# Optimization experiments

Measured on AMD Instinct MI355X. Metric: run time of the kernel, lower is better.

The kernel has to match this reference:

```python
import jax, jax.numpy as jnp
import numpy as np

N, C_IN, C_OUT, HID, H = 4096, 512, 512, 128, 4
HEAD_OUT = C_OUT // H  # 128
MID = 4 * C_OUT        # 2048
R = 1.0                # spatial radius r
L = 48                 # sequence window l
NEG = -1e9


def layer_norm(x, g, b, eps=1e-5):
    m = jnp.mean(x, axis=-1, keepdims=True)
    v = jnp.mean(jnp.square(x - m), axis=-1, keepdims=True)
    return (x - m) * jax.lax.rsqrt(v + eps) * g + b


def setup_inputs() -> dict:
    key = jax.random.key(0)
    ks = jax.random.split(key, 16)
    s = lambda fan: 1.0 / np.sqrt(fan)
    return {
        "x":   jax.random.normal(ks[0], (N, C_IN), jnp.float32),
        "pos": jax.random.normal(ks[1], (N, 3), jnp.float32),
        "ori": jax.random.normal(ks[2], (N, 3), jnp.float32),
        "seq": jnp.arange(N, dtype=jnp.int64) if jax.config.jax_enable_x64 else jnp.arange(N, dtype=jnp.int32),
        "batch": jnp.sort(jax.random.randint(ks[3], (N,), 0, 8)),
        "ln1_g": jnp.ones((C_IN,), jnp.float32),
        "ln1_b": jnp.zeros((C_IN,), jnp.float32),
        "ln2_g": jnp.ones((C_OUT,), jnp.float32),
        "ln2_b": jnp.zeros((C_OUT,), jnp.float32),
        "Wq": jax.random.normal(ks[4], (H, C_IN, HID), jnp.float32) * s(C_IN),
        "Wk": jax.random.normal(ks[5], (H, C_IN, HID), jnp.float32) * s(C_IN),
        "Wv": jax.random.normal(ks[6], (H, C_IN, HID), jnp.float32) * s(C_IN),
        "Wo": jax.random.normal(ks[7], (H, HID, HEAD_OUT), jnp.float32) * s(HID),
        "lnm_g": jnp.ones((MID,), jnp.float32),
        "lnm_b": jnp.zeros((MID,), jnp.float32),
        "W1": jax.random.normal(ks[8], (C_OUT, MID), jnp.float32) * s(C_OUT),
        "W2": jax.random.normal(ks[9], (MID, C_OUT), jnp.float32) * s(MID),
    }


def _block(x, pos, ori, seq, batch, ln1_g, ln1_b, ln2_g, ln2_b,
           Wq, Wk, Wv, Wo, lnm_g, lnm_b, W1, W2):
    identity = x
    xn = layer_norm(x, ln1_g, ln1_b)

    # geometry/sequence neighborhood mask: same graph, ||dp||<=r, |ds|<=l
    d2 = jnp.sum(jnp.square(pos[:, None, :] - pos[None, :, :]), axis=-1)  # [N,N]
    ds = jnp.abs(seq[:, None] - seq[None, :])
    mask = (batch[:, None] == batch[None, :]) & (d2 <= R * R) & (ds <= L)

    # all heads at once (original loops over heads; math identical)
    q = jnp.einsum('nc,hcd->hnd', xn, Wq)
    k = jnp.einsum('nc,hcd->hnd', xn, Wk)
    v = jnp.einsum('nc,hcd->hnd', xn, Wv)
    gbias = ori @ ori.T  # geometric orientation bias [N,N]
    scores = jnp.einsum('hnd,hmd->hnm', q, k) / np.sqrt(HID) + gbias[None]
    scores = jnp.where(mask[None], scores, NEG)
    attn = jax.nn.softmax(scores, axis=-1)
    o = jnp.einsum('hnm,hmd->hnd', attn, v)
    o = jnp.einsum('hnd,hde->hne', o, Wo)               # [H,N,HEAD_OUT]
    o = jnp.transpose(o, (1, 0, 2)).reshape(N, C_OUT)   # concat heads

    x = o + identity
    identity = x
    h = layer_norm(x, ln2_g, ln2_b) @ W1
    h = jax.nn.relu(layer_norm(h, lnm_g, lnm_b))
    return h @ W2 + identity


def reference(x, pos, ori, seq, batch, ln1_g, ln1_b, ln2_g, ln2_b,
              Wq, Wk, Wv, Wo, lnm_g, lnm_b, W1, W2):
    return _block(x, pos, ori, seq, batch, ln1_g, ln1_b, ln2_g, ln2_b,
                  Wq, Wk, Wv, Wo, lnm_g, lnm_b, W1, W2)
```

## Files before the change

kernel.cpp:

```cpp
#include <hip/hip_runtime.h>

typedef unsigned short u16;
typedef unsigned int u32;
typedef float f32x4 __attribute__((ext_vector_type(4)));
typedef __bf16 bf16x8 __attribute__((ext_vector_type(8)));

#define N_TOK 4096
#define QKV_LD 1536
#define NH 4
#define HID 128
#define C_OUT 512

__device__ __forceinline__ float b2f(u16 u) { return __uint_as_float(((u32)u) << 16); }
__device__ __forceinline__ u16 f2b(float f) {
  u32 u = __float_as_uint(f);
  u32 r = (u + 0x7fffu + ((u >> 16) & 1u)) >> 16;
  return (u16)r;
}

__device__ __forceinline__ void gload16(const u16* g, u16* l) {
  __builtin_amdgcn_global_load_lds(
      (const __attribute__((address_space(1))) void*)g,
      (__attribute__((address_space(3))) void*)l, 16, 0, 0);
}

__device__ __forceinline__ void tr32(const float* __restrict__ s,
                                     u16* __restrict__ d, int R, int C,
                                     int r0, int c0, u16 (*tile)[33]) {
  const int tx = threadIdx.x & 31, ty = threadIdx.x >> 5;
#pragma unroll
  for (int i = 0; i < 32; i += 8)
    tile[ty + i][tx] = f2b(s[(size_t)(r0 + ty + i) * C + c0 + tx]);
  __syncthreads();
#pragma unroll
  for (int i = 0; i < 32; i += 8)
    d[(size_t)(c0 + ty + i) * R + r0 + tx] = tile[tx][ty + i];
}

__device__ __forceinline__ void tr32_512(const float* __restrict__ s,
                                         u16* __restrict__ d, int R, int C,
                                         int r0, int c0, u16 (*tile)[33]) {
  const int tx = threadIdx.x & 31, ty = threadIdx.x >> 5;
#pragma unroll
  for (int i = 0; i < 32; i += 16)
    tile[ty + i][tx] = f2b(s[(size_t)(r0 + ty + i) * C + c0 + tx]);
  __syncthreads();
#pragma unroll
  for (int i = 0; i < 32; i += 16)
    d[(size_t)(c0 + ty + i) * R + r0 + tx] = tile[tx][ty + i];
}

__device__ __forceinline__ void ln512_body(
    const float* __restrict__ x, const float* __restrict__ g,
    const float* __restrict__ b, u16* __restrict__ y, int row) {
  const int lane = threadIdx.x & 63;
  const float* xr = x + (size_t)row * 512;
  const int c = lane * 8;
  float4 a0 = *(const float4*)(xr + c);
  float4 a1 = *(const float4*)(xr + c + 4);
  float v[8] = {a0.x, a0.y, a0.z, a0.w, a1.x, a1.y, a1.z, a1.w};
  float s1 = 0.f, s2 = 0.f;
#pragma unroll
  for (int i = 0; i < 8; i++) { s1 += v[i]; s2 += v[i] * v[i]; }
#pragma unroll
  for (int o = 32; o; o >>= 1) { s1 += __shfl_xor(s1, o); s2 += __shfl_xor(s2, o); }
  float mean = s1 * (1.f / 512.f);
  float var = s2 * (1.f / 512.f) - mean * mean;
  float rs = rsqrtf(fmaxf(var, 0.f) + 1e-5f);
  float4 g0 = *(const float4*)(g + c), g1 = *(const float4*)(g + c + 4);
  float4 b0 = *(const float4*)(b + c), b1 = *(const float4*)(b + c + 4);
  float gg[8] = {g0.x, g0.y, g0.z, g0.w, g1.x, g1.y, g1.z, g1.w};
  float bb[8] = {b0.x, b0.y, b0.z, b0.w, b1.x, b1.y, b1.z, b1.w};
  u16 t[8];
#pragma unroll
  for (int i = 0; i < 8; i++) t[i] = f2b((v[i] - mean) * rs * gg[i] + bb[i]);
  *(uint4*)(y + (size_t)row * 512 + c) = *(const uint4*)t;
}

__global__ __launch_bounds__(256) void prep(
    const float* __restrict__ x, const float* __restrict__ ln1g,
    const float* __restrict__ ln1b, u16* __restrict__ xn,
    const float* __restrict__ Wq, const float* __restrict__ Wk,
    const float* __restrict__ Wv, const float* __restrict__ Wo,
    const float* __restrict__ W1,
    u16* __restrict__ Btqkv, u16* __restrict__ Wot, u16* __restrict__ W1t)
{
  __shared__ u16 tile[32][33];
  const int bid = blockIdx.x;
  if (bid < 1024) {
    ln512_body(x, ln1g, ln1b, xn, bid * 4 + (threadIdx.x >> 6));
    return;
  }
  const int idx = bid - 1024;
  const float* s; u16* d; int R, C, r0, c0;
  if (idx < 1024) {
    s = W1; d = W1t; R = 512; C = 2048;
    r0 = (idx >> 6) * 32; c0 = (idx & 63) * 32;
  } else if (idx < 1792) {
    int i = idx - 1024;
    int z = i >> 6, rem = i & 63;
    int which = z >> 2, b = z & 3;
    const float* base = (which == 0) ? Wq : (which == 1) ? Wk : Wv;
    s = base + (size_t)b * 512 * 128;
    d = Btqkv + (size_t)which * 4 * 512 * 128 + (size_t)b * 512 * 128;
    R = 512; C = 128;
    r0 = (rem >> 2) * 32; c0 = (rem & 3) * 32;
  } else {
    int i = idx - 1792;
    int b = i >> 4, rem = i & 15;
    s = Wo + (size_t)b * 128 * 128;
    d = Wot + (size_t)b * 128 * 128;
    R = 128; C = 128;
    r0 = (rem >> 2) * 32; c0 = (rem & 3) * 32;
  }
  tr32(s, d, R, C, r0, c0, tile);
}

__global__ __launch_bounds__(256) void ln512_f32(
    const float* __restrict__ x, const float* __restrict__ g,
    const float* __restrict__ b, u16* __restrict__ y)
{
  ln512_body(x, g, b, y, blockIdx.x * 4 + (threadIdx.x >> 6));
}

__global__ __launch_bounds__(256) void ln2048_bf16_relu(
    const u16* __restrict__ x, const float* __restrict__ g,
    const float* __restrict__ b, u16* __restrict__ y)
{
  const int row = blockIdx.x, tid = threadIdx.x;
  const int c = tid * 8;
  const u16* xr = x + (size_t)row * 2048;
  uint4 u = *(const uint4*)(xr + c);
  u16 e[8]; *(uint4*)e = u;
  float v[8];
#pragma unroll
  for (int i = 0; i < 8; i++) v[i] = b2f(e[i]);
  float s1 = 0.f, s2 = 0.f;
#pragma unroll
  for (int i = 0; i < 8; i++) { s1 += v[i]; s2 += v[i] * v[i]; }
#pragma unroll
  for (int o = 32; o; o >>= 1) { s1 += __shfl_xor(s1, o); s2 += __shfl_xor(s2, o); }
  __shared__ float red[2][4];
  int lane = tid & 63, w = tid >> 6;
  if (lane == 0) { red[0][w] = s1; red[1][w] = s2; }
  __syncthreads();
  s1 = red[0][0] + red[0][1] + red[0][2] + red[0][3];
  s2 = red[1][0] + red[1][1] + red[1][2] + red[1][3];
  float mean = s1 * (1.f / 2048.f);
  float var = s2 * (1.f / 2048.f) - mean * mean;
  float rs = rsqrtf(fmaxf(var, 0.f) + 1e-5f);
  float4 g0 = *(const float4*)(g + c), g1 = *(const float4*)(g + c + 4);
  float4 b0 = *(const float4*)(b + c), b1 = *(const float4*)(b + c + 4);
  float gg[8] = {g0.x, g0.y, g0.z, g0.w, g1.x, g1.y, g1.z, g1.w};
  float bb[8] = {b0.x, b0.y, b0.z, b0.w, b1.x, b1.y, b1.z, b1.w};
  u16 t[8];
#pragma unroll
  for (int i = 0; i < 8; i++)
    t[i] = f2b(fmaxf((v[i] - mean) * rs * gg[i] + bb[i], 0.f));
  *(uint4*)(y + (size_t)row * 2048 + c) = *(const uint4*)t;
}

__global__ __launch_bounds__(512, 4) void gemm128(
    const u16* __restrict__ A, int lda,
    const u16* __restrict__ Bt,
    void* __restrict__ C, int ldc, int outf32,
    const float* __restrict__ res,
    int Kslice, int Ktot, int atomic)
{
  __shared__ u16 As[2][128 * 64];
  __shared__ u16 Bs[2][128 * 64];
  const int id = blockIdx.x + gridDim.x * blockIdx.y;
  const int xr = id & 7, xj = id >> 3;
  const int bm = xr * 4 + (xj & 3);
  const int bn = xj >> 2;
  const int m0 = bm * 128, n0 = bn * 128;
  const int kbase = blockIdx.z * Kslice;
  const int tid = threadIdx.x;
  const int lane = tid & 63, w = tid >> 6;
  const int wm = (w & 1) * 64;
  const int wn = (w >> 1) * 32;
  const int l16 = lane & 15, quad = lane >> 4;

  const int sr = tid >> 3;
  const int sch = (tid & 7) ^ (sr & 7);
  const u16* PA = A + (size_t)(m0 + sr) * lda + kbase + sch * 8;
  const u16* PB = Bt + (size_t)(n0 + sr) * Ktot + kbase + sch * 8;
  const size_t askip = (size_t)64 * lda;
  const size_t bskip = (size_t)64 * Ktot;

  f32x4 acc[4][2];
#pragma unroll
  for (int i = 0; i < 4; i++)
#pragma unroll
    for (int j = 0; j < 2; j++) acc[i][j] = (f32x4){0.f, 0.f, 0.f, 0.f};

  {
    gload16(PA, &As[0][w * 512]);
    gload16(PA + askip, &As[0][4096 + w * 512]);
    gload16(PB, &Bs[0][w * 512]);
    gload16(PB + bskip, &Bs[0][4096 + w * 512]);
  }
  __syncthreads();

  int buf = 0;
  for (int kk = 0; kk < Kslice; kk += 64) {
    if (kk + 64 < Kslice) {
      PA += 64; PB += 64;
      gload16(PA, &As[buf ^ 1][w * 512]);
      gload16(PA + askip, &As[buf ^ 1][4096 + w * 512]);
      gload16(PB, &Bs[buf ^ 1][w * 512]);
      gload16(PB + bskip, &Bs[buf ^ 1][4096 + w * 512]);
    }
#pragma unroll
    for (int kc = 0; kc < 2; kc++) {
      bf16x8 af[4], bfr[2];
#pragma unroll
      for (int mt = 0; mt < 4; mt++) {
        int row = wm + mt * 16 + l16;
        af[mt] = *(const bf16x8*)&As[buf][row * 64 + (((kc * 4 + quad) ^ (row & 7)) * 8)];
      }
#pragma unroll
      for (int nt = 0; nt < 2; nt++) {
        int row = wn + nt * 16 + l16;
        bfr[nt] = *(const bf16x8*)&Bs[buf][row * 64 + (((kc * 4 + quad) ^ (row & 7)) * 8)];
      }
#pragma unroll
      for (int mt = 0; mt < 4; mt++)
#pragma unroll
        for (int nt = 0; nt < 2; nt++)
          acc[mt][nt] = __builtin_amdgcn_mfma_f32_16x16x32_bf16(
              af[mt], bfr[nt], acc[mt][nt], 0, 0, 0);
    }
    __syncthreads();
    buf ^= 1;
  }

#pragma unroll
  for (int mt = 0; mt < 4; mt++)
#pragma unroll
    for (int nt = 0; nt < 2; nt++)
#pragma unroll
      for (int r = 0; r < 4; r++) {
        int gr = m0 + wm + mt * 16 + quad * 4 + r;
        int gc = n0 + wn + nt * 16 + l16;
        size_t off = (size_t)gr * ldc + gc;
        float v = acc[mt][nt][r];
        if (atomic) {
          atomicAdd((float*)C + off, v);
        } else {
          if (res) v += res[off];
          if (outf32) ((float*)C)[off] = v;
          else        ((u16*)C)[off] = f2b(v);
        }
      }
}

#define TQ 32
#define BAND 128
#define KROW 136
#define PROW 132
__global__ __launch_bounds__(512) void attn_mfma(
    const u16* __restrict__ qkv, const float* __restrict__ pos,
    const float* __restrict__ ori, const int* __restrict__ batch,
    const u16* __restrict__ wot, const float* __restrict__ xres,
    float* __restrict__ out,
    const float* __restrict__ W2, u16* __restrict__ W2t)
{
  __shared__ u16 kv[128 * KROW];
  __shared__ u16 qp[TQ * KROW];
  __shared__ float ps[TQ * PROW];
  __shared__ float bpx[BAND], bpy[BAND], bpz[BAND];
  __shared__ float box_[BAND], boy_[BAND], boz_[BAND];
  __shared__ int bb[BAND];

  if (blockIdx.x >= 128) {
    int idx = (blockIdx.x - 128) + blockIdx.y * 256;
    int r0 = (idx >> 4) * 32, c0 = (idx & 15) * 32;
    tr32_512(W2, W2t, 2048, 512, r0, c0, (u16(*)[33])kv);
    return;
  }

  const int h = blockIdx.y;
  const int bxs = (blockIdx.x & 7) * 16 + (blockIdx.x >> 3);
  const int i0 = bxs * TQ;
  const int j0 = i0 - 48;
  const int tid = threadIdx.x;
  const int lane = tid & 63, w = tid >> 6;
  const int l16 = lane & 15, quad = lane >> 4;

  if (tid < BAND) {
    int t = tid, j = j0 + t;
    if (j >= 0 && j < N_TOK) {
      bpx[t] = pos[j * 3 + 0]; bpy[t] = pos[j * 3 + 1]; bpz[t] = pos[j * 3 + 2];
      box_[t] = ori[j * 3 + 0]; boy_[t] = ori[j * 3 + 1]; boz_[t] = ori[j * 3 + 2];
      bb[t] = batch[j];
    } else {
      bpx[t] = bpy[t] = bpz[t] = 0.f;
      box_[t] = boy_[t] = boz_[t] = 0.f;
      bb[t] = -12345;
    }
  }
  for (int idx = tid; idx < BAND * 16; idx += 512) {
    int t = idx >> 4, c8 = (idx & 15) * 8;
    int j = j0 + t;
    int4 val = {0, 0, 0, 0};
    if (j >= 0 && j < N_TOK)
      val = *(const int4*)&qkv[(size_t)j * QKV_LD + 512 + h * HID + c8];
    *(int4*)&kv[t * KROW + c8] = val;
  }
  {
    int q = tid >> 4, c8 = (tid & 15) * 8;
    *(int4*)&qp[q * KROW + c8] =
        *(const int4*)&qkv[(size_t)(i0 + q) * QKV_LD + h * HID + c8];
  }
  __syncthreads();

  {
    bf16x8 bf[4];
#pragma unroll
    for (int kc = 0; kc < 4; kc++)
      bf[kc] = *(const bf16x8*)&kv[(w * 16 + l16) * KROW + kc * 32 + quad * 8];
    const int t = w * 16 + l16;
#pragma unroll
    for (int qt = 0; qt < 2; qt++) {
      bf16x8 af[4];
#pragma unroll
      for (int kc = 0; kc < 4; kc++)
        af[kc] = *(const bf16x8*)&qp[(qt * 16 + l16) * KROW + kc * 32 + quad * 8];
      f32x4 acc = (f32x4){0.f, 0.f, 0.f, 0.f};
#pragma unroll
      for (int kc = 0; kc < 4; kc++)
        acc = __builtin_amdgcn_mfma_f32_16x16x32_bf16(af[kc], bf[kc], acc, 0, 0, 0);
#pragma unroll
      for (int r = 0; r < 4; r++) {
        int q = qt * 16 + quad * 4 + r, iq = q + 48;
        int dseq = iq - t;
        bool ok = (bb[t] == bb[iq]) && (dseq <= 48) && (dseq >= -48);
        {
#pragma clang fp contract(off)
          float dx = bpx[iq] - bpx[t], dy = bpy[iq] - bpy[t], dz = bpz[iq] - bpz[t];
          float d2 = dx * dx + dy * dy + dz * dz;
          ok = ok && (d2 <= 1.0f);
        }
        float s = -1e9f;
        if (ok) {
          float gb = box_[iq] * box_[t] + boy_[iq] * boy_[t] + boz_[iq] * boz_[t];
          s = acc[r] * 0.08838834764831845f + gb;
        }
        ps[q * PROW + t] = s;
      }
    }
  }
  __syncthreads();

  for (int idx = tid; idx < BAND * 32; idx += 512) {
    int t = idx >> 5, d4 = (idx & 31) * 4;
    int j = j0 + t;
    uint2 val; val.x = 0; val.y = 0;
    if (j >= 0 && j < N_TOK)
      val = *(const uint2*)&qkv[(size_t)j * QKV_LD + 1024 + h * HID + d4];
    u16 e[4] = {(u16)val.x, (u16)(val.x >> 16), (u16)val.y, (u16)(val.y >> 16)};
#pragma unroll
    for (int jj = 0; jj < 4; jj++) {
      int dd = (jj + tid) & 3;
      kv[(d4 + dd) * KROW + t] = e[dd];
    }
  }
  {
    int row = tid >> 4, sub = tid & 15;
    float vals[8];
    float m = -1e30f;
#pragma unroll
    for (int i = 0; i < 8; i++) {
      vals[i] = ps[row * PROW + sub + i * 16];
      m = fmaxf(m, vals[i]);
    }
#pragma unroll
    for (int o = 8; o; o >>= 1) m = fmaxf(m, __shfl_xor(m, o));
    float s = 0.f;
#pragma unroll
    for (int i = 0; i < 8; i++) { vals[i] = __expf(vals[i] - m); s += vals[i]; }
#pragma unroll
    for (int o = 8; o; o >>= 1) s += __shfl_xor(s, o);
    float inv = 1.f / s;
#pragma unroll
    for (int i = 0; i < 8; i++)
      qp[row * KROW + sub + i * 16] = f2b(vals[i] * inv);
  }
  __syncthreads();

  u16 obuf[2][4];
  {
    bf16x8 bf[4];
#pragma unroll
    for (int kc = 0; kc < 4; kc++)
      bf[kc] = *(const bf16x8*)&kv[(w * 16 + l16) * KROW + kc * 32 + quad * 8];
#pragma unroll
    for (int qt = 0; qt < 2; qt++) {
      bf16x8 paf[4];
#pragma unroll
      for (int kc = 0; kc < 4; kc++)
        paf[kc] = *(const bf16x8*)&qp[(qt * 16 + l16) * KROW + kc * 32 + quad * 8];
      f32x4 acc = (f32x4){0.f, 0.f, 0.f, 0.f};
#pragma unroll
      for (int kc = 0; kc < 4; kc++)
        acc = __builtin_amdgcn_mfma_f32_16x16x32_bf16(paf[kc], bf[kc], acc, 0, 0, 0);
#pragma unroll
      for (int r = 0; r < 4; r++) obuf[qt][r] = f2b(acc[r]);
    }
  }
  __syncthreads();

#pragma unroll
  for (int qt = 0; qt < 2; qt++) {
#pragma unroll
    for (int r = 0; r < 4; r++)
      qp[(qt * 16 + quad * 4 + r) * KROW + w * 16 + l16] = obuf[qt][r];
  }
  {
    const u16* wsrc = wot + (size_t)h * HID * HID;
    for (int idx = tid; idx < 128 * 16; idx += 512) {
      int e = idx >> 4, c8 = (idx & 15) * 8;
      *(int4*)&kv[e * KROW + c8] = *(const int4*)&wsrc[e * HID + c8];
    }
  }
  __syncthreads();

  {
    bf16x8 bf[4];
#pragma unroll
    for (int kc = 0; kc < 4; kc++)
      bf[kc] = *(const bf16x8*)&kv[(w * 16 + l16) * KROW + kc * 32 + quad * 8];
#pragma unroll
    for (int qt = 0; qt < 2; qt++) {
      bf16x8 oaf[4];
#pragma unroll
      for (int kc = 0; kc < 4; kc++)
        oaf[kc] = *(const bf16x8*)&qp[(qt * 16 + l16) * KROW + kc * 32 + quad * 8];
      f32x4 acc = (f32x4){0.f, 0.f, 0.f, 0.f};
#pragma unroll
      for (int kc = 0; kc < 4; kc++)
        acc = __builtin_amdgcn_mfma_f32_16x16x32_bf16(oaf[kc], bf[kc], acc, 0, 0, 0);
#pragma unroll
      for (int r = 0; r < 4; r++) {
        int q = qt * 16 + quad * 4 + r;
        size_t off = (size_t)(i0 + q) * C_OUT + h * HID + w * 16 + l16;
        out[off] = acc[r] + xres[off];
      }
    }
  }
}

#define MB (1048576)
extern "C" void kernel_launch(void* const* d_in, const int* in_sizes, int n_in,
                              void* d_out, int out_size, void* d_ws, size_t ws_size,
                              hipStream_t stream) {
  const float* x    = (const float*)d_in[0];
  const float* pos  = (const float*)d_in[1];
  const float* ori  = (const float*)d_in[2];
  const int*   batch = (const int*)d_in[4];
  const float* ln1g = (const float*)d_in[5];
  const float* ln1b = (const float*)d_in[6];
  const float* ln2g = (const float*)d_in[7];
  const float* ln2b = (const float*)d_in[8];
  const float* Wq = (const float*)d_in[9];
  const float* Wk = (const float*)d_in[10];
  const float* Wv = (const float*)d_in[11];
  const float* Wo = (const float*)d_in[12];
  const float* lnmg = (const float*)d_in[13];
  const float* lnmb = (const float*)d_in[14];
  const float* W1 = (const float*)d_in[15];
  const float* W2 = (const float*)d_in[16];
  float* out = (float*)d_out;

  char* ws = (char*)d_ws;
  u16* xn    = (u16*)(ws + 0);
  u16* x1n   = (u16*)(ws + 0);
  u16* qkv   = (u16*)(ws + 4 * MB);
  u16* h     = (u16*)(ws + 4 * MB);
  u16* Wot   = (u16*)(ws + 16 * MB);
  u16* Btqkv = (u16*)(ws + 20 * MB);
  u16* W2t   = (u16*)(ws + 20 * MB);
  u16* W1t   = (u16*)(ws + 22 * MB);

  prep<<<dim3(2880), 256, 0, stream>>>(x, ln1g, ln1b, xn,
                                       Wq, Wk, Wv, Wo, W1, Btqkv, Wot, W1t);
  gemm128<<<dim3(12, 32, 1), 512, 0, stream>>>(xn, 512, Btqkv, qkv, QKV_LD, 0,
                                               nullptr, 512, 512, 0);
  attn_mfma<<<dim3(384, NH), 512, 0, stream>>>(qkv, pos, ori, batch, Wot, x, out,
                                               W2, W2t);
  ln512_f32<<<dim3(1024), 256, 0, stream>>>(out, ln2g, ln2b, x1n);
  gemm128<<<dim3(16, 32, 1), 512, 0, stream>>>(x1n, 512, W1t, h, 2048, 0,
                                               nullptr, 512, 512, 0);
  ln2048_bf16_relu<<<dim3(4096), 256, 0, stream>>>(h, lnmg, lnmb, h);
  gemm128<<<dim3(4, 32, 2), 512, 0, stream>>>(h, 2048, W2t, out, 512, 1,
                                              nullptr, 1024, 2048, 1);
}
```

Before: 182.2 us.

## Load K via async global-to-LDS with XOR swizzle and keep Wo in registers

Replaces the padded K/V LDS tile with an unpadded 128-wide tile using an XOR swizzle, filled for K by direct global_load_lds instructions instead of register round-trips. V transpose writes and MFMA operand reads use the same swizzle. The Wo slice for each lane is loaded into registers at kernel start, removing the later LDS staging of Wo and one barrier. The K load drops the in-range guard, so edge blocks read rows outside the token range and rely on masking to discard them.

```diff
diff --git a/kernel.cpp b/kernel.cpp
--- a/kernel.cpp
+++ b/kernel.cpp
@@ -257,7 +257,7 @@
 
 #define TQ 32
 #define BAND 128
-#define KROW 136
+#define QROW 136
 #define PROW 132
 __global__ __launch_bounds__(512) void attn_mfma(
     const u16* __restrict__ qkv, const float* __restrict__ pos,
@@ -266,8 +266,8 @@
     float* __restrict__ out,
     const float* __restrict__ W2, u16* __restrict__ W2t)
 {
-  __shared__ u16 kv[128 * KROW];
-  __shared__ u16 qp[TQ * KROW];
+  __shared__ u16 kv[128 * 128];
+  __shared__ u16 qp[TQ * QROW];
   __shared__ float ps[TQ * PROW];
   __shared__ float bpx[BAND], bpy[BAND], bpz[BAND];
   __shared__ float box_[BAND], boy_[BAND], boz_[BAND];
@@ -287,6 +287,14 @@
   const int tid = threadIdx.x;
   const int lane = tid & 63, w = tid >> 6;
   const int l16 = lane & 15, quad = lane >> 4;
+
+  bf16x8 wof[4];
+  {
+    const u16* wsrc = wot + (size_t)h * HID * HID + (w * 16 + l16) * HID;
+#pragma unroll
+    for (int kc = 0; kc < 4; kc++)
+      wof[kc] = *(const bf16x8*)&wsrc[kc * 32 + quad * 8];
+  }
 
   if (tid < BAND) {
     int t = tid, j = j0 + t;
@@ -300,33 +308,35 @@
       bb[t] = -12345;
     }
   }
-  for (int idx = tid; idx < BAND * 16; idx += 512) {
-    int t = idx >> 4, c8 = (idx & 15) * 8;
-    int j = j0 + t;
-    int4 val = {0, 0, 0, 0};
-    if (j >= 0 && j < N_TOK)
-      val = *(const int4*)&qkv[(size_t)j * QKV_LD + 512 + h * HID + c8];
-    *(int4*)&kv[t * KROW + c8] = val;
+  {
+    const u16* kbase = qkv + 512 + h * HID;
+#pragma unroll
+    for (int call = 0; call < 4; call++) {
+      int row = call * 32 + w * 4 + (lane >> 4);
+      int c = (lane & 15) ^ (row & 15);
+      const u16* g = kbase + (size_t)(j0 + row) * QKV_LD + c * 8;
+      gload16(g, &kv[call * 4096 + w * 512]);
+    }
   }
   {
     int q = tid >> 4, c8 = (tid & 15) * 8;
-    *(int4*)&qp[q * KROW + c8] =
+    *(int4*)&qp[q * QROW + c8] =
         *(const int4*)&qkv[(size_t)(i0 + q) * QKV_LD + h * HID + c8];
   }
   __syncthreads();
 
   {
+    const int t = w * 16 + l16;
     bf16x8 bf[4];
 #pragma unroll
     for (int kc = 0; kc < 4; kc++)
-      bf[kc] = *(const bf16x8*)&kv[(w * 16 + l16) * KROW + kc * 32 + quad * 8];
-    const int t = w * 16 + l16;
+      bf[kc] = *(const bf16x8*)&kv[t * 128 + (((kc * 4 + quad) ^ (t & 15)) * 8)];
 #pragma unroll
     for (int qt = 0; qt < 2; qt++) {
       bf16x8 af[4];
 #pragma unroll
       for (int kc = 0; kc < 4; kc++)
-        af[kc] = *(const bf16x8*)&qp[(qt * 16 + l16) * KROW + kc * 32 + quad * 8];
+        af[kc] = *(const bf16x8*)&qp[(qt * 16 + l16) * QROW + kc * 32 + quad * 8];
       f32x4 acc = (f32x4){0.f, 0.f, 0.f, 0.f};
 #pragma unroll
       for (int kc = 0; kc < 4; kc++)
@@ -360,10 +370,12 @@
     if (j >= 0 && j < N_TOK)
       val = *(const uint2*)&qkv[(size_t)j * QKV_LD + 1024 + h * HID + d4];
     u16 e[4] = {(u16)val.x, (u16)(val.x >> 16), (u16)val.y, (u16)(val.y >> 16)};
+    int ct = t >> 3, cw = t & 7;
 #pragma unroll
     for (int jj = 0; jj < 4; jj++) {
       int dd = (jj + tid) & 3;
-      kv[(d4 + dd) * KROW + t] = e[dd];
+      int d = d4 + dd;
+      kv[d * 128 + ((ct ^ (d & 15)) * 8) + cw] = e[dd];
     }
   }
   {
@@ -385,22 +397,23 @@
     float inv = 1.f / s;
 #pragma unroll
     for (int i = 0; i < 8; i++)
-      qp[row * KROW + sub + i * 16] = f2b(vals[i] * inv);
+      qp[row * QROW + sub + i * 16] = f2b(vals[i] * inv);
   }
   __syncthreads();
 
   u16 obuf[2][4];
   {
+    const int d = w * 16 + l16;
     bf16x8 bf[4];
 #pragma unroll
     for (int kc = 0; kc < 4; kc++)
-      bf[kc] = *(const bf16x8*)&kv[(w * 16 + l16) * KROW + kc * 32 + quad * 8];
+      bf[kc] = *(const bf16x8*)&kv[d * 128 + (((kc * 4 + quad) ^ (d & 15)) * 8)];
 #pragma unroll
     for (int qt = 0; qt < 2; qt++) {
       bf16x8 paf[4];
 #pragma unroll
       for (int kc = 0; kc < 4; kc++)
-        paf[kc] = *(const bf16x8*)&qp[(qt * 16 + l16) * KROW + kc * 32 + quad * 8];
+        paf[kc] = *(const bf16x8*)&qp[(qt * 16 + l16) * QROW + kc * 32 + quad * 8];
       f32x4 acc = (f32x4){0.f, 0.f, 0.f, 0.f};
 #pragma unroll
       for (int kc = 0; kc < 4; kc++)
@@ -415,32 +428,21 @@
   for (int qt = 0; qt < 2; qt++) {
 #pragma unroll
     for (int r = 0; r < 4; r++)
-      qp[(qt * 16 + quad * 4 + r) * KROW + w * 16 + l16] = obuf[qt][r];
-  }
-  {
-    const u16* wsrc = wot + (size_t)h * HID * HID;
-    for (int idx = tid; idx < 128 * 16; idx += 512) {
-      int e = idx >> 4, c8 = (idx & 15) * 8;
-      *(int4*)&kv[e * KROW + c8] = *(const int4*)&wsrc[e * HID + c8];
-    }
-  }
-  __syncthreads();
-
-  {
-    bf16x8 bf[4];
-#pragma unroll
-    for (int kc = 0; kc < 4; kc++)
-      bf[kc] = *(const bf16x8*)&kv[(w * 16 + l16) * KROW + kc * 32 + quad * 8];
+      qp[(qt * 16 + quad * 4 + r) * QROW + w * 16 + l16] = obuf[qt][r];
+  }
+  __syncthreads();
+
+  {
 #pragma unroll
     for (int qt = 0; qt < 2; qt++) {
       bf16x8 oaf[4];
 #pragma unroll
       for (int kc = 0; kc < 4; kc++)
-        oaf[kc] = *(const bf16x8*)&qp[(qt * 16 + l16) * KROW + kc * 32 + quad * 8];
+        oaf[kc] = *(const bf16x8*)&qp[(qt * 16 + l16) * QROW + kc * 32 + quad * 8];
       f32x4 acc = (f32x4){0.f, 0.f, 0.f, 0.f};
 #pragma unroll
       for (int kc = 0; kc < 4; kc++)
-        acc = __builtin_amdgcn_mfma_f32_16x16x32_bf16(oaf[kc], bf[kc], acc, 0, 0, 0);
+        acc = __builtin_amdgcn_mfma_f32_16x16x32_bf16(oaf[kc], wof[kc], acc, 0, 0, 0);
 #pragma unroll
       for (int r = 0; r < 4; r++) {
         int q = qt * 16 + quad * 4 + r;
```

Result: no change. 180.3 us, median of 3 (-1.1%).
